# Kernel tuning notes

Hardware: AMD Instinct MI355X
Metric: run time of the kernel (lower is better)

The kernel has to match this reference:

```python
import jax, jax.numpy as jnp
import numpy as np

L, D, H, N, R = 4, 256, 512, 16, 8  # layers, d_model, hidden=2*d_model, state_dim, dt_rank
OUT_LEN, IN_DIM = 96, 32
EPS = 1e-5


def _layernorm(v, g, b):
    m = jnp.mean(v, axis=-1, keepdims=True)
    var = jnp.mean((v - m) ** 2, axis=-1, keepdims=True)
    return (v - m) / jnp.sqrt(var + EPS) * g + b


def _pos_encoding(T, d):
    pos = jnp.arange(T, dtype=jnp.float32)[:, None]
    div = jnp.exp(jnp.arange(0, d, 2, dtype=jnp.float32) * (-np.log(10000.0) / d))
    pe = jnp.zeros((T, d), dtype=jnp.float32)
    pe = pe.at[:, 0::2].set(jnp.sin(pos * div))
    pe = pe.at[:, 1::2].set(jnp.cos(pos * div))
    return pe


def setup_inputs() -> dict:
    key = jax.random.key(0)
    ks = jax.random.split(key, 20)
    inp = {
        "x": jax.random.normal(ks[0], (8, 1024, IN_DIM), dtype=jnp.float32),
        "emb_w": jax.random.normal(ks[1], (D, IN_DIM), dtype=jnp.float32) * 0.1,
        "emb_b": jnp.zeros((D,), dtype=jnp.float32),
        "norm_g": jnp.ones((L, D), dtype=jnp.float32),
        "norm_b": jnp.zeros((L, D), dtype=jnp.float32),
        "in_w": jax.random.normal(ks[2], (L, H, D), dtype=jnp.float32) * (1.0 / np.sqrt(D)),
        "conv_w": jax.random.normal(ks[3], (L, H, 1, 3), dtype=jnp.float32) * 0.5,
        "A_p": jax.random.normal(ks[4], (L, H, N), dtype=jnp.float32) * 0.01,
        "D_p": jnp.ones((L, H), dtype=jnp.float32),
        "dt1_w": jax.random.normal(ks[5], (L, R, H), dtype=jnp.float32) * (1.0 / np.sqrt(H)),
        "dt1_b": jnp.zeros((L, R), dtype=jnp.float32),
        "dt2_w": jax.random.normal(ks[6], (L, H, R), dtype=jnp.float32) * (1.0 / np.sqrt(R)),
        "dt2_b": jnp.zeros((L, H), dtype=jnp.float32),
        "out_w": jax.random.normal(ks[7], (L, D, H), dtype=jnp.float32) * (1.0 / np.sqrt(H)),
        "final_g": jnp.ones((D,), dtype=jnp.float32),
        "final_b": jnp.zeros((D,), dtype=jnp.float32),
        "head1_w": jax.random.normal(ks[8], (D, D), dtype=jnp.float32) * (1.0 / np.sqrt(D)),
        "head1_b": jnp.zeros((D,), dtype=jnp.float32),
        "head2_w": jax.random.normal(ks[9], (OUT_LEN, D), dtype=jnp.float32) * (1.0 / np.sqrt(D)),
        "head2_b": jnp.zeros((OUT_LEN,), dtype=jnp.float32),
    }
    return inp


def _mamba_block(h, g, b, in_w, conv_w, A_p, D_p, dt1_w, dt1_b, dt2_w, dt2_b, out_w):
    res = h
    v = _layernorm(h, g, b)            # [B,T,D]
    v = jnp.einsum('btd,hd->bth', v, in_w)  # [B,T,H]
    # depthwise conv1d, kernel 3, padding 1, groups=H
    vc = jnp.transpose(v, (0, 2, 1))   # [B,H,T]
    vc = jax.lax.conv_general_dilated(vc, conv_w, window_strides=(1,),
                                      padding=[(1, 1)], feature_group_count=H,
                                      dimension_numbers=('NCH', 'OIH', 'NCH'))
    v = jnp.transpose(jax.nn.silu(vc), (0, 2, 1))  # [B,T,H]
    dt = jax.nn.relu(jnp.einsum('bth,rh->btr', v, dt1_w) + dt1_b)
    dt = jnp.einsum('btr,hr->bth', dt, dt2_w) + dt2_b
    dt = jax.nn.softplus(dt)           # [B,T,H]
    A = -jnp.exp(A_p)                  # [H,N]
    safe_A = jnp.where(jnp.abs(A) < 1e-5, jnp.ones_like(A), A)

    B_sz = v.shape[0]
    state0 = jnp.zeros((B_sz, H, N), dtype=v.dtype)

    def step(state, inp):
        x_t, dt_t = inp  # [B,H] each
        dA = A * dt_t[..., None]            # [B,H,N]
        discA = jnp.exp(dA)
        discB = (discA - 1.0) / safe_A * dt_t[..., None]
        state = discA * state + discB * x_t[..., None]
        y = jnp.einsum('bhn,hn->bh', state, A_p) + D_p * x_t
        return state, y

    xs = (jnp.transpose(v, (1, 0, 2)), jnp.transpose(dt, (1, 0, 2)))  # [T,B,H]
    _, ys = jax.lax.scan(step, state0, xs)
    y = jnp.transpose(ys, (1, 0, 2))   # [B,T,H]
    return res + jnp.einsum('bth,dh->btd', y, out_w)


def reference(x, emb_w, emb_b, norm_g, norm_b, in_w, conv_w, A_p, D_p,
              dt1_w, dt1_b, dt2_w, dt2_b, out_w, final_g, final_b,
              head1_w, head1_b, head2_w, head2_b):
    h = jnp.einsum('bti,di->btd', x, emb_w) + emb_b  # [B,T,D]
    h = h + _pos_encoding(h.shape[1], D)[None]
    for l in range(L):
        h = _mamba_block(h, norm_g[l], norm_b[l], in_w[l], conv_w[l], A_p[l],
                         D_p[l], dt1_w[l], dt1_b[l], dt2_w[l], dt2_b[l], out_w[l])
    h = _layernorm(h, final_g, final_b)
    h = h[:, -1, :]                    # last token [B,D]
    h = jax.nn.silu(h @ head1_w.T + head1_b)
    return h @ head2_w.T + head2_b     # [B, OUT_LEN]
```

## Files before the change

### kernel.cpp

```cpp
#include <hip/hip_runtime.h>
#include <hip/hip_bf16.h>
#include <math.h>

#define BB 8
#define TT 1024
#define DD 256
#define HH 512
#define NN 16
#define RR 8
#define OUT_LEN 96
#define IN_DIM 32
#define MM (BB*TT)

#define SC 32
#define CC (TT/SC)

typedef unsigned short u16;
typedef unsigned int u32;
typedef __attribute__((ext_vector_type(8))) short short8;
typedef __attribute__((ext_vector_type(8))) unsigned short u16x8;
typedef __attribute__((ext_vector_type(4))) float float4v;

__device__ __forceinline__ u16 f2bf(float f) {
    __hip_bfloat16 h = __float2bfloat16(f);
    return *(u16*)&h;
}
__device__ __forceinline__ float bf2f(u16 u) {
    u32 v = ((u32)u) << 16;
    return *(float*)&v;
}

#define GLD_LDS16(src, dst) __builtin_amdgcn_global_load_lds( \
    (const __attribute__((address_space(1))) void*)(src),     \
    (__attribute__((address_space(3))) void*)(dst), 16, 0, 0)

__global__ __launch_bounds__(256) void embed_ln_cvt_kernel(
    const float* __restrict__ x, const float* __restrict__ emb_w,
    const float* __restrict__ emb_b,
    const float* __restrict__ g, const float* __restrict__ b,
    float* __restrict__ h, u16* __restrict__ lnout,
    const float* __restrict__ w_in, u16* __restrict__ wbf_in,
    const float* __restrict__ w_out, u16* __restrict__ wbf_out, int nw)
{
    int bid = blockIdx.x;
    if (bid >= MM) {
        int i = (bid - MM) * 256 + threadIdx.x;
        if (i < nw) wbf_in[i] = f2bf(w_in[i]);
        else        wbf_out[i - nw] = f2bf(w_out[i - nw]);
        return;
    }

    int bt = bid;
    int d  = threadIdx.x;
    int t  = bt & (TT - 1);

    __shared__ float xs[IN_DIM];
    __shared__ float red[4], red2[4];
    if (threadIdx.x < IN_DIM) xs[threadIdx.x] = x[bt * IN_DIM + threadIdx.x];
    __syncthreads();

    const float* w = emb_w + d * IN_DIM;
    float acc = emb_b[d];
#pragma unroll
    for (int i = 0; i < IN_DIM; i++) acc = fmaf(xs[i], w[i], acc);

    int i2 = d & ~1;
    float div = expf(-(float)i2 * (logf(10000.0f) / (float)DD));
    float arg = (float)t * div;
    float pe = (d & 1) ? cosf(arg) : sinf(arg);
    float val = acc + pe;
    h[bt * DD + d] = val;

    float s = val;
#pragma unroll
    for (int o = 32; o > 0; o >>= 1) s += __shfl_down(s, o);
    int lane = d & 63, wave = d >> 6;
    if (lane == 0) red[wave] = s;
    __syncthreads();
    float mean = (red[0] + red[1] + red[2] + red[3]) * (1.0f / DD);

    float c = val - mean;
    float s2 = c * c;
#pragma unroll
    for (int o = 32; o > 0; o >>= 1) s2 += __shfl_down(s2, o);
    if (lane == 0) red2[wave] = s2;
    __syncthreads();
    float var = (red2[0] + red2[1] + red2[2] + red2[3]) * (1.0f / DD);

    lnout[bt * DD + d] = f2bf(c * rsqrtf(var + 1e-5f) * g[d] + b[d]);
}

template<int BM, int BN, int OUT_BF16>
__global__ __launch_bounds__(256) void gemm_bf16(
    const u16* __restrict__ A, const u16* __restrict__ B,
    void* __restrict__ Cv, int M, int N, int K, int addC)
{
    constexpr int BK = 64;
    constexpr int MT = BM / 32;
    constexpr int NT = BN / 32;
    static_assert(BN == 64, "B staging assumes BN==64");

    __shared__ __align__(16) u16 Al[8][BM][8];
    __shared__ __align__(16) u16 Bl[8][BN][8];

    const int tid = threadIdx.x;
    const int bm = blockIdx.y * BM;
    const int bn = blockIdx.x * BN;
    const int wid = tid >> 6, lane = tid & 63;
    const int wm = wid >> 1, wn = wid & 1;
    const int lq = lane >> 4, lm = lane & 15;

    float4v acc[MT][NT];
#pragma unroll
    for (int i = 0; i < MT; i++)
#pragma unroll
        for (int j = 0; j < NT; j++) acc[i][j] = (float4v){0.f, 0.f, 0.f, 0.f};

    for (int k0 = 0; k0 < K; k0 += BK) {
#pragma unroll
        for (int it = 0; it < (8 * BM) / 256; it++) {
            int c = it * 256 + tid;
            int q = c / BM, row = c % BM;
            GLD_LDS16(A + (size_t)(bm + row) * K + k0 + q * 8, &Al[q][row][0]);
        }
#pragma unroll
        for (int it = 0; it < (8 * BN) / 256; it++) {
            int c = it * 256 + tid;
            int q = c / BN, row = c % BN;
            GLD_LDS16(B + (size_t)(bn + row) * K + k0 + q * 8, &Bl[q][row][0]);
        }
        __syncthreads();

        short8 af[2][MT], bf[2][NT];
#pragma unroll
        for (int kk = 0; kk < 2; kk++) {
#pragma unroll
            for (int mt = 0; mt < MT; mt++)
                af[kk][mt] = *(const short8*)&Al[kk * 4 + lq][wm * (BM / 2) + mt * 16 + lm][0];
#pragma unroll
            for (int nt = 0; nt < NT; nt++)
                bf[kk][nt] = *(const short8*)&Bl[kk * 4 + lq][wn * (BN / 2) + nt * 16 + lm][0];
        }

#pragma unroll
        for (int kk = 0; kk < 2; kk++)
#pragma unroll
            for (int mt = 0; mt < MT; mt++)
#pragma unroll
                for (int nt = 0; nt < NT; nt++)
                    acc[mt][nt] = __builtin_amdgcn_mfma_f32_16x16x32_bf16(
                        af[kk][mt], bf[kk][nt], acc[mt][nt], 0, 0, 0);
        __syncthreads();
    }

#pragma unroll
    for (int mt = 0; mt < MT; mt++)
#pragma unroll
        for (int nt = 0; nt < NT; nt++) {
            int row0 = bm + wm * (BM / 2) + mt * 16 + lq * 4;
            int col  = bn + wn * (BN / 2) + nt * 16 + lm;
#pragma unroll
            for (int r = 0; r < 4; r++) {
                float vv = acc[mt][nt][r];
                if (OUT_BF16) {
                    ((u16*)Cv)[(size_t)(row0 + r) * N + col] = f2bf(vv);
                } else {
                    float* cp = (float*)Cv + (size_t)(row0 + r) * N + col;
                    if (addC) vv += *cp;
                    *cp = vv;
                }
            }
        }
}

__global__ __launch_bounds__(256) void gemm2_ln(
    const u16* __restrict__ A, const u16* __restrict__ B,
    float* __restrict__ h,
    const float* __restrict__ g, const float* __restrict__ bb,
    u16* __restrict__ lnout, int doLN)
{
    constexpr int BM = 32;
    __shared__ __align__(16) u16 Al[8][BM][8];
    __shared__ __align__(16) u16 Bl[8][256][8];
    __shared__ float rs[2][BM], qs[2][BM];

    const int tid = threadIdx.x;
    const int bm = blockIdx.x * BM;
    const int wid = tid >> 6, lane = tid & 63;
    const int wm = wid >> 1, wn = wid & 1;
    const int lq = lane >> 4, lm = lane & 15;

    float4v acc[8];
#pragma unroll
    for (int j = 0; j < 8; j++) acc[j] = (float4v){0.f, 0.f, 0.f, 0.f};

    for (int k0 = 0; k0 < 512; k0 += 64) {
        {
            int q = tid >> 5, row = tid & 31;
            GLD_LDS16(A + (size_t)(bm + row) * 512 + k0 + q * 8, &Al[q][row][0]);
        }
#pragma unroll
        for (int it = 0; it < 8; it++) {
            int c = it * 256 + tid;
            int q = c >> 8, row = c & 255;
            GLD_LDS16(B + (size_t)row * 512 + k0 + q * 8, &Bl[q][row][0]);
        }
        __syncthreads();

        short8 af[2], bf[2][8];
#pragma unroll
        for (int kk = 0; kk < 2; kk++) {
            af[kk] = *(const short8*)&Al[kk * 4 + lq][wm * 16 + lm][0];
#pragma unroll
            for (int nt = 0; nt < 8; nt++)
                bf[kk][nt] = *(const short8*)&Bl[kk * 4 + lq][wn * 128 + nt * 16 + lm][0];
        }
#pragma unroll
        for (int kk = 0; kk < 2; kk++)
#pragma unroll
            for (int nt = 0; nt < 8; nt++)
                acc[nt] = __builtin_amdgcn_mfma_f32_16x16x32_bf16(
                    af[kk], bf[kk][nt], acc[nt], 0, 0, 0);
        __syncthreads();
    }

    float val[4][8];
    float s1[4] = {0.f, 0.f, 0.f, 0.f}, s2[4] = {0.f, 0.f, 0.f, 0.f};
#pragma unroll
    for (int r = 0; r < 4; r++) {
        int row = bm + wm * 16 + lq * 4 + r;
#pragma unroll
        for (int nt = 0; nt < 8; nt++) {
            int col = wn * 128 + nt * 16 + lm;
            float v = acc[nt][r] + h[(size_t)row * DD + col];
            val[r][nt] = v;
            s1[r] += v;
            s2[r] = fmaf(v, v, s2[r]);
            h[(size_t)row * DD + col] = v;
        }
    }
#pragma unroll
    for (int r = 0; r < 4; r++) {
#pragma unroll
        for (int o = 1; o < 16; o <<= 1) {
            s1[r] += __shfl_xor(s1[r], o);
            s2[r] += __shfl_xor(s2[r], o);
        }
    }
    if (lm == 0) {
#pragma unroll
        for (int r = 0; r < 4; r++) {
            rs[wn][wm * 16 + lq * 4 + r] = s1[r];
            qs[wn][wm * 16 + lq * 4 + r] = s2[r];
        }
    }
    __syncthreads();

    if (doLN) {
#pragma unroll
        for (int r = 0; r < 4; r++) {
            int i = wm * 16 + lq * 4 + r;
            int row = bm + i;
            float mean = (rs[0][i] + rs[1][i]) * (1.0f / DD);
            float var  = (qs[0][i] + qs[1][i]) * (1.0f / DD) - mean * mean;
            float rstd = rsqrtf(var + 1e-5f);
#pragma unroll
            for (int nt = 0; nt < 8; nt++) {
                int col = wn * 128 + nt * 16 + lm;
                lnout[(size_t)row * DD + col] =
                    f2bf((val[r][nt] - mean) * rstd * g[col] + bb[col]);
            }
        }
    }
}

__global__ __launch_bounds__(256) void conv_dt1_kernel(
    const u16* __restrict__ v, const float* __restrict__ cwg,
    const float* __restrict__ w1g, const float* __restrict__ b1g,
    u16* __restrict__ vsb, float* __restrict__ dtr)
{
    __shared__ float w1s[RR * 2 * 256];
    int tid = threadIdx.x;
    {
        int lane = tid & 63, rc = tid >> 6;
#pragma unroll
        for (int i = 0; i < 4; i++) {
            int rci = rc + i * 4;
            int r = rci >> 1, jc = rci & 1;
            float4 wv = *(const float4*)(w1g + r * HH + lane * 8 + jc * 4);
            *(float4*)&w1s[rci * 256 + lane * 4] = wv;
        }
    }
    __syncthreads();

    int wave = tid >> 6, lane = tid & 63;
    int m = blockIdx.x * 4 + wave;
    int t = m & (TT - 1);
    int h0 = lane * 8;

    const u16* vrow = v + (size_t)m * HH + h0;
    u16x8 x0 = *(const u16x8*)vrow;
    u16x8 xm = (t > 0)      ? *(const u16x8*)(vrow - HH) : (u16x8)(0);
    u16x8 xp = (t < TT - 1) ? *(const u16x8*)(vrow + HH) : (u16x8)(0);

    const float* wp = cwg + h0 * 3;
    float a[8];
    u16x8 o;
#pragma unroll
    for (int j = 0; j < 8; j++) {
        float s = wp[j * 3] * bf2f(xm[j]);
        s = fmaf(wp[j * 3 + 1], bf2f(x0[j]), s);
        s = fmaf(wp[j * 3 + 2], bf2f(xp[j]), s);
        s = s / (1.0f + __expf(-s));
        a[j] = s;
        o[j] = f2bf(s);
    }
    *(u16x8*)(vsb + (size_t)m * HH + h0) = o;

    float acc[RR];
#pragma unroll
    for (int r = 0; r < RR; r++) {
        float4 wlo = *(const float4*)&w1s[(r * 2 + 0) * 256 + lane * 4];
        float4 whi = *(const float4*)&w1s[(r * 2 + 1) * 256 + lane * 4];
        float s = a[0] * wlo.x;
        s = fmaf(a[1], wlo.y, s);
        s = fmaf(a[2], wlo.z, s);
        s = fmaf(a[3], wlo.w, s);
        s = fmaf(a[4], whi.x, s);
        s = fmaf(a[5], whi.y, s);
        s = fmaf(a[6], whi.z, s);
        s = fmaf(a[7], whi.w, s);
        acc[r] = s;
    }
#pragma unroll
    for (int r = 0; r < RR; r++) {
#pragma unroll
        for (int o2 = 1; o2 < 64; o2 <<= 1) acc[r] += __shfl_xor(acc[r], o2);
    }
    if (lane == 0) {
#pragma unroll
        for (int r = 0; r < RR; r++) acc[r] = fmaxf(acc[r] + b1g[r], 0.0f);
        *(float4*)(dtr + (size_t)m * RR)     = make_float4(acc[0], acc[1], acc[2], acc[3]);
        *(float4*)(dtr + (size_t)m * RR + 4) = make_float4(acc[4], acc[5], acc[6], acc[7]);
    }
}

__device__ __forceinline__ float softplus_f(float s) {
    return (s > 20.0f) ? s : __logf(1.0f + __expf(s));
}

__global__ __launch_bounds__(256) void scan_pass1(
    const u16* __restrict__ vs, const float* __restrict__ dtr,
    const float* __restrict__ dt2_w, const float* __restrict__ dt2_b,
    const float* __restrict__ A_p,
    u16* __restrict__ Lst, float* __restrict__ sdt)
{
    int h = blockIdx.x * 256 + threadIdx.x;
    int c = blockIdx.y;
    int b = blockIdx.z;

    float A[NN], invA[NN], st[NN];
    const float* ap = A_p + h * NN;
#pragma unroll
    for (int n = 0; n < NN; n++) {
        float a = -__expf(ap[n]);
        A[n] = a; invA[n] = 1.0f / a; st[n] = 0.0f;
    }
    float w2[RR];
#pragma unroll
    for (int r = 0; r < RR; r++) w2[r] = dt2_w[h * RR + r];
    float b2 = dt2_b[h];

    const u16*   vbase = vs  + ((size_t)b * TT + (size_t)c * SC) * HH + h;
    const float* drow  = dtr + ((size_t)b * TT + (size_t)c * SC) * RR;

    float dr[RR];
#pragma unroll
    for (int r = 0; r < RR; r++) dr[r] = drow[r];

    float s_dt = 0.0f;
#pragma unroll 2
    for (int t = 0; t < SC; t++) {
        float drn[RR];
        if (t + 1 < SC) {
#pragma unroll
            for (int r = 0; r < RR; r++) drn[r] = drow[(t + 1) * RR + r];
        }
        float s = b2;
#pragma unroll
        for (int r = 0; r < RR; r++) s = fmaf(dr[r], w2[r], s);
        float dt = softplus_f(s);
        float xv = bf2f(vbase[(size_t)t * HH]);
        s_dt += dt;
#pragma unroll
        for (int n = 0; n < NN; n++) {
            float e  = __expf(A[n] * dt);
            float dB = (e - 1.0f) * invA[n] * dt;
            st[n] = fmaf(e, st[n], dB * xv);
        }
#pragma unroll
        for (int r = 0; r < RR; r++) dr[r] = drn[r];
    }

    size_t base = (((size_t)c * BB + b) * HH + h) * NN;
    u16x8 lo, hi;
#pragma unroll
    for (int n = 0; n < 8; n++) { lo[n] = f2bf(st[n]); hi[n] = f2bf(st[n + 8]); }
    *(u16x8*)(Lst + base)     = lo;
    *(u16x8*)(Lst + base + 8) = hi;
    sdt[((size_t)c * BB + b) * HH + h] = s_dt;
}

__global__ __launch_bounds__(256) void scan_carry(
    const float* __restrict__ A_p, const float* __restrict__ sdt,
    u16* __restrict__ Lst)
{
    int i = blockIdx.x * 256 + threadIdx.x;
    int n  = i & (NN - 1);
    int bh = i >> 4;
    int h  = bh & (HH - 1);
    int b  = bh >> 9;

    float A = -__expf(A_p[h * NN + n]);
    float E = 0.0f;
    for (int c = 0; c < CC; c++) {
        size_t sidx = ((size_t)c * BB + b) * HH + h;
        float P = __expf(A * sdt[sidx]);
        size_t lidx = sidx * NN + n;
        float Lc = bf2f(Lst[lidx]);
        Lst[lidx] = f2bf(E);
        E = fmaf(P, E, Lc);
    }
}

__global__ __launch_bounds__(256) void scan_pass2(
    const u16* __restrict__ vs,
    const float* __restrict__ dtr,
    const float* __restrict__ dt2_w,
    const float* __restrict__ dt2_b,
    const float* __restrict__ A_p, const float* __restrict__ D_p,
    const u16* __restrict__ carry,
    u16* __restrict__ y)
{
    int h = blockIdx.x * 256 + threadIdx.x;
    int c = blockIdx.y;
    int b = blockIdx.z;

    float A[NN], invA[NN], Ap[NN], st[NN];
    const float* app = A_p + h * NN;
    size_t cbase = (((size_t)c * BB + b) * HH + h) * NN;
    {
        u16x8 lo = *(const u16x8*)(carry + cbase);
        u16x8 hi = *(const u16x8*)(carry + cbase + 8);
#pragma unroll
        for (int n = 0; n < 8; n++) { st[n] = bf2f(lo[n]); st[n + 8] = bf2f(hi[n]); }
    }
#pragma unroll
    for (int n = 0; n < NN; n++) {
        float apv = app[n];
        Ap[n] = apv;
        float a = -__expf(apv);
        A[n] = a; invA[n] = 1.0f / a;
    }
    float w2[RR];
#pragma unroll
    for (int r = 0; r < RR; r++) w2[r] = dt2_w[h * RR + r];
    float b2 = dt2_b[h];
    float Dp = D_p[h];

    const u16*   vbase = vs  + ((size_t)b * TT + (size_t)c * SC) * HH + h;
    const float* drow  = dtr + ((size_t)b * TT + (size_t)c * SC) * RR;
    u16*         ybase = y   + ((size_t)b * TT + (size_t)c * SC) * HH + h;

    float dr[RR];
#pragma unroll
    for (int r = 0; r < RR; r++) dr[r] = drow[r];

#pragma unroll 2
    for (int t = 0; t < SC; t++) {
        float drn[RR];
        if (t + 1 < SC) {
#pragma unroll
            for (int r = 0; r < RR; r++) drn[r] = drow[(t + 1) * RR + r];
        }
        float s = b2;
#pragma unroll
        for (int r = 0; r < RR; r++) s = fmaf(dr[r], w2[r], s);
        float dt = softplus_f(s);
        float xv = bf2f(vbase[(size_t)t * HH]);
        float acc = Dp * xv;
#pragma unroll
        for (int n = 0; n < NN; n++) {
            float e  = __expf(A[n] * dt);
            float dB = (e - 1.0f) * invA[n] * dt;
            st[n] = fmaf(e, st[n], dB * xv);
            acc = fmaf(st[n], Ap[n], acc);
        }
        ybase[(size_t)t * HH] = f2bf(acc);
#pragma unroll
        for (int r = 0; r < RR; r++) dr[r] = drn[r];
    }
}

__global__ __launch_bounds__(256) void head_kernel(
    const float* __restrict__ h,
    const float* __restrict__ fg, const float* __restrict__ fb,
    const float* __restrict__ w1, const float* __restrict__ b1,
    const float* __restrict__ w2, const float* __restrict__ b2,
    float* __restrict__ out)
{
    int b = blockIdx.x;
    int d = threadIdx.x;
    __shared__ float hn[DD], s1[DD];
    __shared__ float red[4];

    float v = h[((size_t)b * TT + (TT - 1)) * DD + d];

    float s = v;
#pragma unroll
    for (int o = 32; o > 0; o >>= 1) s += __shfl_down(s, o);
    int lane = d & 63, wave = d >> 6;
    if (lane == 0) red[wave] = s;
    __syncthreads();
    float mean = (red[0] + red[1] + red[2] + red[3]) * (1.0f / DD);
    __syncthreads();

    float c = v - mean;
    float s2 = c * c;
#pragma unroll
    for (int o = 32; o > 0; o >>= 1) s2 += __shfl_down(s2, o);
    if (lane == 0) red[wave] = s2;
    __syncthreads();
    float var = (red[0] + red[1] + red[2] + red[3]) * (1.0f / DD);

    hn[d] = c * rsqrtf(var + 1e-5f) * fg[d] + fb[d];
    __syncthreads();

    float a1 = b1[d];
    const float* w1r = w1 + d * DD;
#pragma unroll 8
    for (int k = 0; k < DD; k++) a1 = fmaf(hn[k], w1r[k], a1);
    s1[d] = a1 / (1.0f + __expf(-a1));
    __syncthreads();

    if (d < OUT_LEN) {
        float a2 = b2[d];
        const float* w2r = w2 + d * DD;
#pragma unroll 8
        for (int k = 0; k < DD; k++) a2 = fmaf(s1[k], w2r[k], a2);
        out[b * OUT_LEN + d] = a2;
    }
}

extern "C" void kernel_launch(void* const* d_in, const int* in_sizes, int n_in,
                              void* d_out, int out_size, void* d_ws, size_t ws_size,
                              hipStream_t stream)
{
    (void)in_sizes; (void)n_in; (void)out_size; (void)ws_size;

    const float* x       = (const float*)d_in[0];
    const float* emb_w   = (const float*)d_in[1];
    const float* emb_b   = (const float*)d_in[2];
    const float* norm_g  = (const float*)d_in[3];
    const float* norm_b  = (const float*)d_in[4];
    const float* in_w    = (const float*)d_in[5];
    const float* conv_w  = (const float*)d_in[6];
    const float* A_p     = (const float*)d_in[7];
    const float* D_p     = (const float*)d_in[8];
    const float* dt1_w   = (const float*)d_in[9];
    const float* dt1_b   = (const float*)d_in[10];
    const float* dt2_w   = (const float*)d_in[11];
    const float* dt2_b   = (const float*)d_in[12];
    const float* out_w   = (const float*)d_in[13];
    const float* final_g = (const float*)d_in[14];
    const float* final_b = (const float*)d_in[15];
    const float* head1_w = (const float*)d_in[16];
    const float* head1_b = (const float*)d_in[17];
    const float* head2_w = (const float*)d_in[18];
    const float* head2_b = (const float*)d_in[19];
    float* outp = (float*)d_out;

    char* ws = (char*)d_ws;
    float* h     = (float*)ws;                ws += (size_t)MM * DD * 4;
    u16*   vbf   = (u16*)ws;                  ws += (size_t)MM * HH * 2;
    u16*   vsb   = (u16*)ws;                  ws += (size_t)MM * HH * 2;
    u16*   ybf   = (u16*)ws;                  ws += (size_t)MM * HH * 2;
    u16*   lnbuf = (u16*)ws;                  ws += (size_t)MM * DD * 2;
    float* dtr   = (float*)ws;                ws += (size_t)MM * RR * 4;
    u16*   Lst   = (u16*)ws;                  ws += (size_t)CC * BB * HH * NN * 2;
    float* sdt   = (float*)ws;                ws += (size_t)CC * BB * HH * 4;
    u16*   wbf_in  = (u16*)ws;                ws += (size_t)4 * HH * DD * 2;
    u16*   wbf_out = (u16*)ws;                ws += (size_t)4 * DD * HH * 2;

    const int NW = 4 * HH * DD;
    embed_ln_cvt_kernel<<<MM + (2 * NW) / 256, 256, 0, stream>>>(
        x, emb_w, emb_b, norm_g, norm_b, h, lnbuf,
        in_w, wbf_in, out_w, wbf_out, NW);

    for (int l = 0; l < 4; l++) {
        gemm_bf16<128, 64, 1><<<dim3(HH / 64, MM / 128), 256, 0, stream>>>(
            lnbuf, wbf_in + (size_t)l * HH * DD, vbf, MM, HH, DD, 0);
        conv_dt1_kernel<<<MM / 4, 256, 0, stream>>>(
            vbf, conv_w + (size_t)l * HH * 3,
            dt1_w + (size_t)l * RR * HH, dt1_b + l * RR, vsb, dtr);

        scan_pass1<<<dim3(HH / 256, CC, BB), 256, 0, stream>>>(
            vsb, dtr, dt2_w + (size_t)l * HH * RR, dt2_b + l * HH,
            A_p + (size_t)l * HH * NN, Lst, sdt);
        scan_carry<<<(BB * HH * NN) / 256, 256, 0, stream>>>(
            A_p + (size_t)l * HH * NN, sdt, Lst);
        scan_pass2<<<dim3(HH / 256, CC, BB), 256, 0, stream>>>(
            vsb, dtr, dt2_w + (size_t)l * HH * RR, dt2_b + l * HH,
            A_p + (size_t)l * HH * NN, D_p + l * HH, Lst, ybf);

        const float* g_next = (l < 3) ? (norm_g + (l + 1) * DD) : final_g;
        const float* b_next = (l < 3) ? (norm_b + (l + 1) * DD) : final_b;
        gemm2_ln<<<MM / 32, 256, 0, stream>>>(
            ybf, wbf_out + (size_t)l * DD * HH, h, g_next, b_next,
            lnbuf, (l < 3) ? 1 : 0);
    }

    head_kernel<<<BB, 256, 0, stream>>>(h, final_g, final_b,
                                        head1_w, head1_b, head2_w, head2_b, outp);
}
```

Baseline: 501.0 us.

## Halve scan chunk size and simplify per-step state update math

Scan chunks shrink from 32 to 16 timesteps, doubling the number of chunk-parallel blocks in both scan passes while lengthening the serial carry loop. The per-step dt-projection inputs are staged once per block in shared memory, and the next x value is prefetched one step ahead. The inner state update uses a raw exp2 with a pre-scaled A and an algebraically refactored form, e*(st+u)-u, which removes a multiply per state element. The carry kernel also prefetches the next chunk's values, and launch bounds request four blocks per CU.

```diff
diff --git a/kernel.cpp b/kernel.cpp
--- a/kernel.cpp
+++ b/kernel.cpp
@@ -12,7 +12,7 @@
 #define IN_DIM 32
 #define MM (BB*TT)
 
-#define SC 32
+#define SC 16
 #define CC (TT/SC)
 
 typedef unsigned short u16;
@@ -349,7 +349,7 @@
     return (s > 20.0f) ? s : __logf(1.0f + __expf(s));
 }
 
-__global__ __launch_bounds__(256) void scan_pass1(
+__global__ __launch_bounds__(256, 4) void scan_pass1(
     const u16* __restrict__ vs, const float* __restrict__ dtr,
     const float* __restrict__ dt2_w, const float* __restrict__ dt2_b,
     const float* __restrict__ A_p,
@@ -359,47 +359,47 @@
     int c = blockIdx.y;
     int b = blockIdx.z;
 
-    float A[NN], invA[NN], st[NN];
+    __shared__ float ds[SC * RR];
+    {
+        const float* drow = dtr + ((size_t)b * TT + (size_t)c * SC) * RR;
+        if (threadIdx.x < SC * RR) ds[threadIdx.x] = drow[threadIdx.x];
+    }
+
+    float A2[NN], invA[NN], st[NN];
     const float* ap = A_p + h * NN;
 #pragma unroll
     for (int n = 0; n < NN; n++) {
         float a = -__expf(ap[n]);
-        A[n] = a; invA[n] = 1.0f / a; st[n] = 0.0f;
+        A2[n] = a * 1.44269504f;
+        invA[n] = 1.0f / a;
+        st[n] = 0.0f;
     }
     float w2[RR];
 #pragma unroll
     for (int r = 0; r < RR; r++) w2[r] = dt2_w[h * RR + r];
     float b2 = dt2_b[h];
 
-    const u16*   vbase = vs  + ((size_t)b * TT + (size_t)c * SC) * HH + h;
-    const float* drow  = dtr + ((size_t)b * TT + (size_t)c * SC) * RR;
-
-    float dr[RR];
-#pragma unroll
-    for (int r = 0; r < RR; r++) dr[r] = drow[r];
+    const u16* vbase = vs + ((size_t)b * TT + (size_t)c * SC) * HH + h;
+    float xv = bf2f(vbase[0]);
+    __syncthreads();
 
     float s_dt = 0.0f;
 #pragma unroll 2
     for (int t = 0; t < SC; t++) {
-        float drn[RR];
-        if (t + 1 < SC) {
-#pragma unroll
-            for (int r = 0; r < RR; r++) drn[r] = drow[(t + 1) * RR + r];
-        }
+        float xn = (t + 1 < SC) ? bf2f(vbase[(size_t)(t + 1) * HH]) : 0.0f;
         float s = b2;
 #pragma unroll
-        for (int r = 0; r < RR; r++) s = fmaf(dr[r], w2[r], s);
+        for (int r = 0; r < RR; r++) s = fmaf(ds[t * RR + r], w2[r], s);
         float dt = softplus_f(s);
-        float xv = bf2f(vbase[(size_t)t * HH]);
         s_dt += dt;
+        float dtx = dt * xv;
 #pragma unroll
         for (int n = 0; n < NN; n++) {
-            float e  = __expf(A[n] * dt);
-            float dB = (e - 1.0f) * invA[n] * dt;
-            st[n] = fmaf(e, st[n], dB * xv);
-        }
-#pragma unroll
-        for (int r = 0; r < RR; r++) dr[r] = drn[r];
+            float e = __builtin_amdgcn_exp2f(A2[n] * dt);
+            float u = invA[n] * dtx;
+            st[n] = fmaf(e, st[n] + u, -u);
+        }
+        xv = xn;
     }
 
     size_t base = (((size_t)c * BB + b) * HH + h) * NN;
@@ -423,17 +423,26 @@
 
     float A = -__expf(A_p[h * NN + n]);
     float E = 0.0f;
+    size_t sidx = (size_t)b * HH + h;
+    const size_t stride = (size_t)BB * HH;
+    float sd = sdt[sidx];
+    u16 Lu = Lst[sidx * NN + n];
     for (int c = 0; c < CC; c++) {
-        size_t sidx = ((size_t)c * BB + b) * HH + h;
-        float P = __expf(A * sdt[sidx]);
-        size_t lidx = sidx * NN + n;
-        float Lc = bf2f(Lst[lidx]);
-        Lst[lidx] = f2bf(E);
+        float nsd = 0.0f; u16 nLu = 0;
+        if (c + 1 < CC) {
+            size_t nidx = sidx + stride;
+            nsd = sdt[nidx];
+            nLu = Lst[nidx * NN + n];
+        }
+        float P = __expf(A * sd);
+        float Lc = bf2f(Lu);
+        Lst[sidx * NN + n] = f2bf(E);
         E = fmaf(P, E, Lc);
-    }
-}
-
-__global__ __launch_bounds__(256) void scan_pass2(
+        sidx += stride; sd = nsd; Lu = nLu;
+    }
+}
+
+__global__ __launch_bounds__(256, 4) void scan_pass2(
     const u16* __restrict__ vs,
     const float* __restrict__ dtr,
     const float* __restrict__ dt2_w,
@@ -446,7 +455,13 @@
     int c = blockIdx.y;
     int b = blockIdx.z;
 
-    float A[NN], invA[NN], Ap[NN], st[NN];
+    __shared__ float ds[SC * RR];
+    {
+        const float* drow = dtr + ((size_t)b * TT + (size_t)c * SC) * RR;
+        if (threadIdx.x < SC * RR) ds[threadIdx.x] = drow[threadIdx.x];
+    }
+
+    float A2[NN], invA[NN], Ap[NN], st[NN];
     const float* app = A_p + h * NN;
     size_t cbase = (((size_t)c * BB + b) * HH + h) * NN;
     {
@@ -460,7 +475,8 @@
         float apv = app[n];
         Ap[n] = apv;
         float a = -__expf(apv);
-        A[n] = a; invA[n] = 1.0f / a;
+        A2[n] = a * 1.44269504f;
+        invA[n] = 1.0f / a;
     }
     float w2[RR];
 #pragma unroll
@@ -468,37 +484,29 @@
     float b2 = dt2_b[h];
     float Dp = D_p[h];
 
-    const u16*   vbase = vs  + ((size_t)b * TT + (size_t)c * SC) * HH + h;
-    const float* drow  = dtr + ((size_t)b * TT + (size_t)c * SC) * RR;
-    u16*         ybase = y   + ((size_t)b * TT + (size_t)c * SC) * HH + h;
-
-    float dr[RR];
-#pragma unroll
-    for (int r = 0; r < RR; r++) dr[r] = drow[r];
+    const u16* vbase = vs + ((size_t)b * TT + (size_t)c * SC) * HH + h;
+    u16*       ybase = y  + ((size_t)b * TT + (size_t)c * SC) * HH + h;
+    float xv = bf2f(vbase[0]);
+    __syncthreads();
 
 #pragma unroll 2
     for (int t = 0; t < SC; t++) {
-        float drn[RR];
-        if (t + 1 < SC) {
-#pragma unroll
-            for (int r = 0; r < RR; r++) drn[r] = drow[(t + 1) * RR + r];
-        }
+        float xn = (t + 1 < SC) ? bf2f(vbase[(size_t)(t + 1) * HH]) : 0.0f;
         float s = b2;
 #pragma unroll
-        for (int r = 0; r < RR; r++) s = fmaf(dr[r], w2[r], s);
+        for (int r = 0; r < RR; r++) s = fmaf(ds[t * RR + r], w2[r], s);
         float dt = softplus_f(s);
-        float xv = bf2f(vbase[(size_t)t * HH]);
+        float dtx = dt * xv;
         float acc = Dp * xv;
 #pragma unroll
         for (int n = 0; n < NN; n++) {
-            float e  = __expf(A[n] * dt);
-            float dB = (e - 1.0f) * invA[n] * dt;
-            st[n] = fmaf(e, st[n], dB * xv);
+            float e = __builtin_amdgcn_exp2f(A2[n] * dt);
+            float u = invA[n] * dtx;
+            st[n] = fmaf(e, st[n] + u, -u);
             acc = fmaf(st[n], Ap[n], acc);
         }
         ybase[(size_t)t * HH] = f2bf(acc);
-#pragma unroll
-        for (int r = 0; r < RR; r++) dr[r] = drn[r];
+        xv = xn;
     }
 }
 
```

Result: faster. 486.0 us (-3.0%).
